# Performance work log

Measured on AMD Instinct MI355X. Metric: run time of the kernel, lower is better.

The kernel has to match this reference:

```python
import jax, jax.numpy as jnp
import numpy as np

DIM = 1024
HEADS = 16
DIM_HEAD = 64
INNER = HEADS * DIM_HEAD  # 1024
EPS = 1e-5


def setup_inputs() -> dict:
    key = jax.random.key(0)
    ks = jax.random.split(key, 8)
    B, N = 4, 2048
    s = 0.02
    return {
        "query": jax.random.normal(ks[0], (B, N, DIM), jnp.float32),
        "key_": jax.random.normal(ks[1], (B, N, DIM), jnp.float32),
        "value": jax.random.normal(ks[2], (B, N, DIM), jnp.float32),
        "Wq": jax.random.normal(ks[3], (DIM, INNER), jnp.float32) * s,
        "Wk": jax.random.normal(ks[4], (DIM, INNER), jnp.float32) * s,
        "Wv": jax.random.normal(ks[5], (DIM, INNER), jnp.float32) * s,
        "Wo": jax.random.normal(ks[6], (INNER, DIM), jnp.float32) * s,
        "bo": jnp.zeros((DIM,), jnp.float32),
        "gamma": jnp.ones((DIM,), jnp.float32),
        "beta": jnp.zeros((DIM,), jnp.float32),
    }


def reference(query, key_, value, Wq, Wk, Wv, Wo, bo, gamma, beta):
    B, N, _ = query.shape
    scale = DIM_HEAD ** (-0.5)
    # project and split heads: [B, H, N, Dh]
    q = (query @ Wq).reshape(B, N, HEADS, DIM_HEAD).transpose(0, 2, 1, 3)
    k = (key_ @ Wk).reshape(B, N, HEADS, DIM_HEAD).transpose(0, 2, 1, 3)
    v = (value @ Wv).reshape(B, N, HEADS, DIM_HEAD).transpose(0, 2, 1, 3)
    dots = jnp.einsum("bhnd,bhmd->bhnm", q, k) * scale  # [B,H,N,N]
    attn = jax.nn.softmax(dots, axis=-1)
    out = jnp.einsum("bhnm,bhmd->bhnd", attn, v)
    out = out.transpose(0, 2, 1, 3).reshape(B, N, INNER)
    out = out @ Wo + bo  # dropout p=0.0 is identity
    # LayerNorm over last dim
    mu = out.mean(-1, keepdims=True)
    var = ((out - mu) ** 2).mean(-1, keepdims=True)
    normed = (out - mu) * jax.lax.rsqrt(var + EPS) * gamma + beta
    return normed + query
```

## Files before the change

### kernel.cpp

```cpp
#include <hip/hip_runtime.h>
#include <stdint.h>

#define K_DIM 1024
#define B_SZ 4
#define N_SEQ 2048
#define HEADS 16
#define DH 64
#define M_TOT (B_SZ * N_SEQ)

typedef __bf16 bf16x8 __attribute__((ext_vector_type(8)));
typedef __bf16 bf16x4 __attribute__((ext_vector_type(4)));
typedef float f32x4 __attribute__((ext_vector_type(4)));

typedef const uint32_t __attribute__((address_space(1))) gas_u32;
typedef uint32_t __attribute__((address_space(3))) las_u32;

#define CE_SCALE 0.1803368801f

__device__ __forceinline__ uint16_t f2bf(float f) {
  uint32_t u = __float_as_uint(f);
  u += 0x7FFFu + ((u >> 16) & 1u);
  return (uint16_t)(u >> 16);
}

__device__ __forceinline__ void gld_lds16(const uint16_t* g, uint16_t* lds) {
  __builtin_amdgcn_global_load_lds((gas_u32*)g, (las_u32*)lds, 16, 0, 0);
}

__global__ __launch_bounds__(256) void conv_bf16_k(const float* __restrict__ s0,
                                                   const float* __restrict__ s1,
                                                   const float* __restrict__ s2,
                                                   uint16_t* __restrict__ dstbase, int n4) {
  const int z = blockIdx.y;
  const float* src = (z == 0) ? s0 : (z == 1) ? s1 : s2;
  uint16_t* dst = dstbase + (size_t)z * M_TOT * K_DIM;
  int i = blockIdx.x * blockDim.x + threadIdx.x;
  if (i < n4) {
    float4 v = ((const float4*)src)[i];
    ushort4 o;
    o.x = f2bf(v.x); o.y = f2bf(v.y); o.z = f2bf(v.z); o.w = f2bf(v.w);
    ((ushort4*)dst)[i] = o;
  }
}

__global__ __launch_bounds__(256) void transpose_conv(const float* __restrict__ s0,
                                                      const float* __restrict__ s1,
                                                      const float* __restrict__ s2,
                                                      const float* __restrict__ s3,
                                                      uint16_t* __restrict__ dstbase) {
  __shared__ float tile[32][33];
  const int z = blockIdx.z;
  const float* src = (z == 0) ? s0 : (z == 1) ? s1 : (z == 2) ? s2 : s3;
  uint16_t* dst = dstbase + (size_t)z * 1024 * 1024;
  const int tx = threadIdx.x, ty = threadIdx.y;
  const int bx = blockIdx.x * 32, by = blockIdx.y * 32;
#pragma unroll
  for (int i = 0; i < 32; i += 8)
    tile[ty + i][tx] = src[(size_t)(by + ty + i) * 1024 + bx + tx];
  __syncthreads();
#pragma unroll
  for (int i = 0; i < 32; i += 8)
    dst[(size_t)(bx + ty + i) * 1024 + by + tx] = f2bf(tile[tx][ty + i]);
}

template <int MODE>
__global__ __launch_bounds__(256, 2) void gemm_bf16(const uint16_t* __restrict__ A,
                                                    const uint16_t* __restrict__ BT,
                                                    void* __restrict__ Cout,
                                                    const float* __restrict__ bias) {
  __shared__ __align__(16) uint16_t As[128 * 32];
  __shared__ __align__(16) uint16_t Bs[128 * 32];
  const int tid = threadIdx.x;
  const int wave = tid >> 6, lane = tid & 63;
  const int g = lane >> 4, c16 = lane & 15;
  const int m0 = blockIdx.y * 128, n0 = blockIdx.x * 128;
  const int wr = wave >> 1, wc = wave & 1;
  float scale = 1.f;
  if (MODE == 0) {
    const int z = blockIdx.z;
    A += (size_t)z * M_TOT * K_DIM;
    BT += (size_t)z * 1024 * 1024;
    Cout = (void*)((uint16_t*)Cout + (size_t)z * M_TOT * K_DIM);
    scale = (z == 0) ? CE_SCALE : 1.f;
  }

  const f32x4 fzero = {0.f, 0.f, 0.f, 0.f};
  f32x4 acc[4][4];
#pragma unroll
  for (int i = 0; i < 4; ++i)
#pragma unroll
    for (int j = 0; j < 4; ++j) acc[i][j] = fzero;

  const int srow = wave * 32 + (lane >> 2);
  const int scol = (lane & 3) * 8;
  const uint16_t* ag0 = A + (size_t)(m0 + srow) * K_DIM + scol;
  const uint16_t* ag1 = A + (size_t)(m0 + srow + 16) * K_DIM + scol;
  const uint16_t* bg0 = BT + (size_t)(n0 + srow) * K_DIM + scol;
  const uint16_t* bg1 = BT + (size_t)(n0 + srow + 16) * K_DIM + scol;
  uint16_t* la0 = &As[(wave * 32) * 32];
  uint16_t* la1 = &As[(wave * 32 + 16) * 32];
  uint16_t* lb0 = &Bs[(wave * 32) * 32];
  uint16_t* lb1 = &Bs[(wave * 32 + 16) * 32];

  for (int kt = 0; kt < K_DIM / 32; ++kt) {
    __syncthreads();
    gld_lds16(ag0 + kt * 32, la0);
    gld_lds16(ag1 + kt * 32, la1);
    gld_lds16(bg0 + kt * 32, lb0);
    gld_lds16(bg1 + kt * 32, lb1);
    __syncthreads();
    bf16x8 avec[4], bvec[4];
#pragma unroll
    for (int i = 0; i < 4; ++i)
      avec[i] = *(const bf16x8*)&As[(wr * 64 + i * 16 + c16) * 32 + g * 8];
#pragma unroll
    for (int j = 0; j < 4; ++j)
      bvec[j] = *(const bf16x8*)&Bs[(wc * 64 + j * 16 + c16) * 32 + g * 8];
#pragma unroll
    for (int i = 0; i < 4; ++i)
#pragma unroll
      for (int j = 0; j < 4; ++j)
        acc[i][j] = __builtin_amdgcn_mfma_f32_16x16x32_bf16(avec[i], bvec[j], acc[i][j], 0, 0, 0);
  }

#pragma unroll
  for (int i = 0; i < 4; ++i) {
#pragma unroll
    for (int j = 0; j < 4; ++j) {
      const int col = n0 + wc * 64 + j * 16 + c16;
      if (MODE == 2) {
        const int h = col >> 6, d = col & 63;
        const int row0 = m0 + wr * 64 + i * 16 + g * 4;
        const int b = row0 >> 11, n = row0 & 2047;
        ushort4 o;
        o.x = f2bf(acc[i][j][0]); o.y = f2bf(acc[i][j][1]);
        o.z = f2bf(acc[i][j][2]); o.w = f2bf(acc[i][j][3]);
        *(ushort4*)&((uint16_t*)Cout)[(((size_t)(b * HEADS + h)) * DH + d) * N_SEQ + n] = o;
      } else {
#pragma unroll
        for (int r = 0; r < 4; ++r) {
          const int row = m0 + wr * 64 + i * 16 + g * 4 + r;
          if (MODE == 0) {
            const int b = row >> 11, n = row & 2047;
            const int h = col >> 6, d = col & 63;
            ((uint16_t*)Cout)[(((size_t)(b * HEADS + h)) * N_SEQ + n) * DH + d] =
                f2bf(acc[i][j][r] * scale);
          } else {
            ((float*)Cout)[(size_t)row * 1024 + col] = acc[i][j][r] + bias[col];
          }
        }
      }
    }
  }
}

__global__ __launch_bounds__(256, 4) void attention_k(const uint16_t* __restrict__ qm,
                                                      const uint16_t* __restrict__ km,
                                                      const uint16_t* __restrict__ vtm,
                                                      uint16_t* __restrict__ om) {
  __shared__ __align__(16) uint16_t Ks[64 * 64];
  __shared__ __align__(16) uint16_t Vs[64 * 64];
  __shared__ __align__(16) uint16_t Pt[4][32 * 64];
  const int tid = threadIdx.x;
  const int wave = tid >> 6, lane = tid & 63;
  const int g = lane >> 4, c16 = lane & 15;
  const int bh = blockIdx.y, b = bh >> 4, h = bh & 15;
  const int q0 = blockIdx.x * 128 + wave * 32;

  const uint16_t* qbase = qm + (size_t)bh * N_SEQ * DH;
  const uint16_t* kbase = km + (size_t)bh * N_SEQ * DH;
  const uint16_t* vbase = vtm + (size_t)bh * DH * N_SEQ;

  bf16x8 qf[2][2];
#pragma unroll
  for (int qc = 0; qc < 2; ++qc) {
    const uint16_t* qp = qbase + (size_t)(q0 + qc * 16 + c16) * DH + g * 8;
    qf[qc][0] = *(const bf16x8*)qp;
    qf[qc][1] = *(const bf16x8*)(qp + 32);
  }

  const f32x4 fz = {0.f, 0.f, 0.f, 0.f};
  f32x4 oacc[2][4];
#pragma unroll
  for (int qc = 0; qc < 2; ++qc)
#pragma unroll
    for (int jt = 0; jt < 4; ++jt) oacc[qc][jt] = fz;
  float l[2] = {0.f, 0.f};

  uint16_t* ptw = Pt[wave];
  const int sw = c16 & 7;

  for (int t = 0; t < N_SEQ / 64; ++t) {
    __syncthreads();
#pragma unroll
    for (int p = 0; p < 2; ++p) {
      const int idx = p * 256 + tid;
      {
        const int e = idx * 8, row = e >> 6, ch = idx & 7;
        *(uint4*)&Ks[row * 64 + ((ch ^ (row & 7)) << 3)] =
            *(const uint4*)&kbase[(size_t)t * 4096 + e];
      }
      {
        const int vr = idx >> 3, ch = idx & 7;
        *(uint4*)&Vs[vr * 64 + ((ch ^ (vr & 7)) << 3)] =
            *(const uint4*)&vbase[(size_t)vr * N_SEQ + t * 64 + ch * 8];
      }
    }
    __syncthreads();

#pragma unroll
    for (int kt = 0; kt < 4; ++kt) {
      const int krow = kt * 16 + c16;
      bf16x8 kf0 = *(const bf16x8*)&Ks[krow * 64 + ((g ^ sw) << 3)];
      bf16x8 kf1 = *(const bf16x8*)&Ks[krow * 64 + (((4 + g) ^ sw) << 3)];
#pragma unroll
      for (int qc = 0; qc < 2; ++qc) {
        f32x4 z = fz;
        z = __builtin_amdgcn_mfma_f32_16x16x32_bf16(kf0, qf[qc][0], z, 0, 0, 0);
        z = __builtin_amdgcn_mfma_f32_16x16x32_bf16(kf1, qf[qc][1], z, 0, 0, 0);
        const float p0 = __builtin_amdgcn_exp2f(z[0]);
        const float p1 = __builtin_amdgcn_exp2f(z[1]);
        const float p2 = __builtin_amdgcn_exp2f(z[2]);
        const float p3 = __builtin_amdgcn_exp2f(z[3]);
        l[qc] += (p0 + p1) + (p2 + p3);
        bf16x4 pk;
        pk[0] = (__bf16)p0; pk[1] = (__bf16)p1; pk[2] = (__bf16)p2; pk[3] = (__bf16)p3;
        *(bf16x4*)&ptw[(qc * 16 + c16) * 64 + (((kt * 2 + (g >> 1)) ^ sw) << 3) + (g & 1) * 4] = pk;
      }
    }

#pragma unroll
    for (int kc = 0; kc < 2; ++kc) {
      bf16x8 pa[2];
#pragma unroll
      for (int qc = 0; qc < 2; ++qc)
        pa[qc] = *(const bf16x8*)&ptw[(qc * 16 + c16) * 64 + (((kc * 4 + g) ^ sw) << 3)];
#pragma unroll
      for (int jt = 0; jt < 4; ++jt) {
        const int vrow = jt * 16 + c16;
        bf16x8 vb = *(const bf16x8*)&Vs[vrow * 64 + (((kc * 4 + g) ^ sw) << 3)];
#pragma unroll
        for (int qc = 0; qc < 2; ++qc)
          oacc[qc][jt] = __builtin_amdgcn_mfma_f32_16x16x32_bf16(pa[qc], vb, oacc[qc][jt], 0, 0, 0);
      }
    }
  }

#pragma unroll
  for (int qc = 0; qc < 2; ++qc) {
    l[qc] += __shfl_xor(l[qc], 16);
    l[qc] += __shfl_xor(l[qc], 32);
  }

#pragma unroll
  for (int qc = 0; qc < 2; ++qc) {
#pragma unroll
    for (int r = 0; r < 4; ++r) {
      const float lr = __shfl(l[qc], g * 4 + r, 16);
      const float inv = 1.f / lr;
      const int row = q0 + qc * 16 + g * 4 + r;
      const size_t base = ((size_t)b * N_SEQ + row) * 1024 + h * 64;
#pragma unroll
      for (int jt = 0; jt < 4; ++jt)
        om[base + jt * 16 + c16] = f2bf(oacc[qc][jt][r] * inv);
    }
  }
}

__global__ __launch_bounds__(256) void ln_res_k(const float* __restrict__ proj,
                                                const float* __restrict__ query,
                                                const float* __restrict__ gamma,
                                                const float* __restrict__ beta,
                                                float* __restrict__ out) {
  const int row = blockIdx.x;
  const int tid = threadIdx.x;
  const size_t base = (size_t)row * 1024 + tid * 4;
  float4 v = *(const float4*)(proj + base);
  float s = v.x + v.y + v.z + v.w;
  float s2 = v.x * v.x + v.y * v.y + v.z * v.z + v.w * v.w;
#pragma unroll
  for (int off = 1; off < 64; off <<= 1) {
    s += __shfl_xor(s, off);
    s2 += __shfl_xor(s2, off);
  }
  __shared__ float red[8];
  const int wave = tid >> 6, lane = tid & 63;
  if (lane == 0) { red[wave] = s; red[4 + wave] = s2; }
  __syncthreads();
  s = red[0] + red[1] + red[2] + red[3];
  s2 = red[4] + red[5] + red[6] + red[7];
  const float mu = s * (1.f / 1024.f);
  const float var = fmaxf(s2 * (1.f / 1024.f) - mu * mu, 0.f);
  const float rstd = rsqrtf(var + 1e-5f);
  float4 gq = *(const float4*)(gamma + tid * 4);
  float4 bq = *(const float4*)(beta + tid * 4);
  float4 qq = *(const float4*)(query + base);
  float4 o;
  o.x = (v.x - mu) * rstd * gq.x + bq.x + qq.x;
  o.y = (v.y - mu) * rstd * gq.y + bq.y + qq.y;
  o.z = (v.z - mu) * rstd * gq.z + bq.z + qq.z;
  o.w = (v.w - mu) * rstd * gq.w + bq.w + qq.w;
  *(float4*)(out + base) = o;
}

extern "C" void kernel_launch(void* const* d_in, const int* in_sizes, int n_in,
                              void* d_out, int out_size, void* d_ws, size_t ws_size,
                              hipStream_t stream) {
  (void)in_sizes; (void)n_in; (void)out_size; (void)ws_size;
  const float* query = (const float*)d_in[0];
  const float* key_ = (const float*)d_in[1];
  const float* value = (const float*)d_in[2];
  const float* Wq = (const float*)d_in[3];
  const float* Wk = (const float*)d_in[4];
  const float* Wv = (const float*)d_in[5];
  const float* Wo = (const float*)d_in[6];
  const float* bo = (const float*)d_in[7];
  const float* gamma = (const float*)d_in[8];
  const float* beta = (const float*)d_in[9];
  float* out = (float*)d_out;

  const size_t NELEM = (size_t)M_TOT * 1024;
  uint16_t* wsp = (uint16_t*)d_ws;
  uint16_t* WqT = wsp;
  uint16_t* WvT = WqT + 2 * 1024 * 1024;
  uint16_t* WoT = WqT + 3 * 1024 * 1024;
  uint16_t* xq = WqT + 4 * 1024 * 1024;
  uint16_t* xv = xq + 2 * NELEM;
  uint16_t* qb = xq + 3 * NELEM;
  uint16_t* vt = qb + 2 * NELEM;
  uint16_t* attnO = xq;
  float* proj = (float*)(xq + NELEM);

  const int n4 = (int)(NELEM / 4);
  conv_bf16_k<<<dim3(8192, 3), 256, 0, stream>>>(query, key_, value, xq, n4);

  transpose_conv<<<dim3(32, 32, 4), dim3(32, 8), 0, stream>>>(Wq, Wk, Wv, Wo, WqT);

  gemm_bf16<0><<<dim3(8, 64, 2), 256, 0, stream>>>(xq, WqT, qb, nullptr);
  gemm_bf16<2><<<dim3(8, 64), 256, 0, stream>>>(xv, WvT, vt, nullptr);

  attention_k<<<dim3(N_SEQ / 128, 64), 256, 0, stream>>>(qb, qb + NELEM, vt, attnO);

  gemm_bf16<1><<<dim3(8, 64), 256, 0, stream>>>(attnO, WoT, proj, bo);

  ln_res_k<<<8192, 256, 0, stream>>>(proj, query, gamma, beta, out);
}
```

Before: 374.2 us.

## Merge QKV projections into one launch and prefetch K/V tiles in attention

The Q, K and V projection GEMMs now run as a single launch with three z-slices, and V is written transposed from the third slice. This removes one kernel launch and its tail. The attention kernel now handles 64 query rows per wave (256 per block), so each K/V tile loaded into shared memory is reused across twice as many queries. It also prefetches the next K/V tile into registers during compute, which overlaps global loads with MFMA work. In exchange it uses more registers and shared memory, lowers launch bounds to 2 blocks per CU, and launches half as many attention blocks.

```diff
diff --git a/kernel.cpp b/kernel.cpp
--- a/kernel.cpp
+++ b/kernel.cpp
@@ -75,12 +75,12 @@
   const int g = lane >> 4, c16 = lane & 15;
   const int m0 = blockIdx.y * 128, n0 = blockIdx.x * 128;
   const int wr = wave >> 1, wc = wave & 1;
+  int z = 0;
   float scale = 1.f;
-  if (MODE == 0) {
-    const int z = blockIdx.z;
+  if (MODE == 3) {
+    z = blockIdx.z;
     A += (size_t)z * M_TOT * K_DIM;
     BT += (size_t)z * 1024 * 1024;
-    Cout = (void*)((uint16_t*)Cout + (size_t)z * M_TOT * K_DIM);
     scale = (z == 0) ? CE_SCALE : 1.f;
   }
 
@@ -128,22 +128,24 @@
 #pragma unroll
     for (int j = 0; j < 4; ++j) {
       const int col = n0 + wc * 64 + j * 16 + c16;
-      if (MODE == 2) {
+      if (MODE == 3 && z == 2) {
         const int h = col >> 6, d = col & 63;
         const int row0 = m0 + wr * 64 + i * 16 + g * 4;
         const int b = row0 >> 11, n = row0 & 2047;
         ushort4 o;
         o.x = f2bf(acc[i][j][0]); o.y = f2bf(acc[i][j][1]);
         o.z = f2bf(acc[i][j][2]); o.w = f2bf(acc[i][j][3]);
-        *(ushort4*)&((uint16_t*)Cout)[(((size_t)(b * HEADS + h)) * DH + d) * N_SEQ + n] = o;
+        *(ushort4*)&((uint16_t*)Cout)[(size_t)2 * M_TOT * 1024 +
+                                      (((size_t)(b * HEADS + h)) * DH + d) * N_SEQ + n] = o;
       } else {
 #pragma unroll
         for (int r = 0; r < 4; ++r) {
           const int row = m0 + wr * 64 + i * 16 + g * 4 + r;
-          if (MODE == 0) {
+          if (MODE == 3) {
             const int b = row >> 11, n = row & 2047;
             const int h = col >> 6, d = col & 63;
-            ((uint16_t*)Cout)[(((size_t)(b * HEADS + h)) * N_SEQ + n) * DH + d] =
+            ((uint16_t*)Cout)[(size_t)z * M_TOT * 1024 +
+                              (((size_t)(b * HEADS + h)) * N_SEQ + n) * DH + d] =
                 f2bf(acc[i][j][r] * scale);
           } else {
             ((float*)Cout)[(size_t)row * 1024 + col] = acc[i][j][r] + bias[col];
@@ -154,67 +156,76 @@
   }
 }
 
-__global__ __launch_bounds__(256, 4) void attention_k(const uint16_t* __restrict__ qm,
+__global__ __launch_bounds__(256, 2) void attention_k(const uint16_t* __restrict__ qm,
                                                       const uint16_t* __restrict__ km,
                                                       const uint16_t* __restrict__ vtm,
                                                       uint16_t* __restrict__ om) {
   __shared__ __align__(16) uint16_t Ks[64 * 64];
   __shared__ __align__(16) uint16_t Vs[64 * 64];
-  __shared__ __align__(16) uint16_t Pt[4][32 * 64];
+  __shared__ __align__(16) uint16_t Pt[4][64 * 64];
   const int tid = threadIdx.x;
   const int wave = tid >> 6, lane = tid & 63;
   const int g = lane >> 4, c16 = lane & 15;
   const int bh = blockIdx.y, b = bh >> 4, h = bh & 15;
-  const int q0 = blockIdx.x * 128 + wave * 32;
+  const int q0 = blockIdx.x * 256 + wave * 64;
 
   const uint16_t* qbase = qm + (size_t)bh * N_SEQ * DH;
   const uint16_t* kbase = km + (size_t)bh * N_SEQ * DH;
   const uint16_t* vbase = vtm + (size_t)bh * DH * N_SEQ;
 
-  bf16x8 qf[2][2];
-#pragma unroll
-  for (int qc = 0; qc < 2; ++qc) {
+  bf16x8 qf[4][2];
+#pragma unroll
+  for (int qc = 0; qc < 4; ++qc) {
     const uint16_t* qp = qbase + (size_t)(q0 + qc * 16 + c16) * DH + g * 8;
     qf[qc][0] = *(const bf16x8*)qp;
     qf[qc][1] = *(const bf16x8*)(qp + 32);
   }
 
   const f32x4 fz = {0.f, 0.f, 0.f, 0.f};
-  f32x4 oacc[2][4];
-#pragma unroll
-  for (int qc = 0; qc < 2; ++qc)
+  f32x4 oacc[4][4];
+#pragma unroll
+  for (int qc = 0; qc < 4; ++qc)
 #pragma unroll
     for (int jt = 0; jt < 4; ++jt) oacc[qc][jt] = fz;
-  float l[2] = {0.f, 0.f};
+  float l[4] = {0.f, 0.f, 0.f, 0.f};
 
   uint16_t* ptw = Pt[wave];
   const int sw = c16 & 7;
 
+  const int ch = tid & 7;
+  const int krow0 = tid >> 3, krow1 = (256 + tid) >> 3;
+  const int kdst0 = krow0 * 64 + ((ch ^ (krow0 & 7)) << 3);
+  const int kdst1 = krow1 * 64 + ((ch ^ (krow1 & 7)) << 3);
+
+  uint4 kp0, kp1, vp0, vp1;
+  kp0 = *(const uint4*)&kbase[(size_t)tid * 8];
+  kp1 = *(const uint4*)&kbase[(size_t)(256 + tid) * 8];
+  vp0 = *(const uint4*)&vbase[(size_t)krow0 * N_SEQ + ch * 8];
+  vp1 = *(const uint4*)&vbase[(size_t)krow1 * N_SEQ + ch * 8];
+  *(uint4*)&Ks[kdst0] = kp0;
+  *(uint4*)&Ks[kdst1] = kp1;
+  *(uint4*)&Vs[kdst0] = vp0;
+  *(uint4*)&Vs[kdst1] = vp1;
+  __syncthreads();
+
   for (int t = 0; t < N_SEQ / 64; ++t) {
-    __syncthreads();
-#pragma unroll
-    for (int p = 0; p < 2; ++p) {
-      const int idx = p * 256 + tid;
-      {
-        const int e = idx * 8, row = e >> 6, ch = idx & 7;
-        *(uint4*)&Ks[row * 64 + ((ch ^ (row & 7)) << 3)] =
-            *(const uint4*)&kbase[(size_t)t * 4096 + e];
-      }
-      {
-        const int vr = idx >> 3, ch = idx & 7;
-        *(uint4*)&Vs[vr * 64 + ((ch ^ (vr & 7)) << 3)] =
-            *(const uint4*)&vbase[(size_t)vr * N_SEQ + t * 64 + ch * 8];
-      }
-    }
-    __syncthreads();
+    if (t < N_SEQ / 64 - 1) {
+      const size_t ko = (size_t)(t + 1) * 4096;
+      const int vc = (t + 1) * 64;
+      kp0 = *(const uint4*)&kbase[ko + (size_t)tid * 8];
+      kp1 = *(const uint4*)&kbase[ko + (size_t)(256 + tid) * 8];
+      vp0 = *(const uint4*)&vbase[(size_t)krow0 * N_SEQ + vc + ch * 8];
+      vp1 = *(const uint4*)&vbase[(size_t)krow1 * N_SEQ + vc + ch * 8];
+    }
 
 #pragma unroll
     for (int kt = 0; kt < 4; ++kt) {
       const int krow = kt * 16 + c16;
       bf16x8 kf0 = *(const bf16x8*)&Ks[krow * 64 + ((g ^ sw) << 3)];
       bf16x8 kf1 = *(const bf16x8*)&Ks[krow * 64 + (((4 + g) ^ sw) << 3)];
-#pragma unroll
-      for (int qc = 0; qc < 2; ++qc) {
+      const int pcol = (((kt * 2 + (g >> 1)) ^ sw) << 3) + (g & 1) * 4;
+#pragma unroll
+      for (int qc = 0; qc < 4; ++qc) {
         f32x4 z = fz;
         z = __builtin_amdgcn_mfma_f32_16x16x32_bf16(kf0, qf[qc][0], z, 0, 0, 0);
         z = __builtin_amdgcn_mfma_f32_16x16x32_bf16(kf1, qf[qc][1], z, 0, 0, 0);
@@ -225,35 +236,44 @@
         l[qc] += (p0 + p1) + (p2 + p3);
         bf16x4 pk;
         pk[0] = (__bf16)p0; pk[1] = (__bf16)p1; pk[2] = (__bf16)p2; pk[3] = (__bf16)p3;
-        *(bf16x4*)&ptw[(qc * 16 + c16) * 64 + (((kt * 2 + (g >> 1)) ^ sw) << 3) + (g & 1) * 4] = pk;
+        *(bf16x4*)&ptw[(qc * 16 + c16) * 64 + pcol] = pk;
       }
     }
 
 #pragma unroll
     for (int kc = 0; kc < 2; ++kc) {
-      bf16x8 pa[2];
-#pragma unroll
-      for (int qc = 0; qc < 2; ++qc)
-        pa[qc] = *(const bf16x8*)&ptw[(qc * 16 + c16) * 64 + (((kc * 4 + g) ^ sw) << 3)];
+      const int fcol = ((kc * 4 + g) ^ sw) << 3;
+      bf16x8 pa[4];
+#pragma unroll
+      for (int qc = 0; qc < 4; ++qc)
+        pa[qc] = *(const bf16x8*)&ptw[(qc * 16 + c16) * 64 + fcol];
 #pragma unroll
       for (int jt = 0; jt < 4; ++jt) {
-        const int vrow = jt * 16 + c16;
-        bf16x8 vb = *(const bf16x8*)&Vs[vrow * 64 + (((kc * 4 + g) ^ sw) << 3)];
-#pragma unroll
-        for (int qc = 0; qc < 2; ++qc)
+        bf16x8 vb = *(const bf16x8*)&Vs[(jt * 16 + c16) * 64 + fcol];
+#pragma unroll
+        for (int qc = 0; qc < 4; ++qc)
           oacc[qc][jt] = __builtin_amdgcn_mfma_f32_16x16x32_bf16(pa[qc], vb, oacc[qc][jt], 0, 0, 0);
       }
     }
-  }
-
-#pragma unroll
-  for (int qc = 0; qc < 2; ++qc) {
+
+    if (t < N_SEQ / 64 - 1) {
+      __syncthreads();
+      *(uint4*)&Ks[kdst0] = kp0;
+      *(uint4*)&Ks[kdst1] = kp1;
+      *(uint4*)&Vs[kdst0] = vp0;
+      *(uint4*)&Vs[kdst1] = vp1;
+      __syncthreads();
+    }
+  }
+
+#pragma unroll
+  for (int qc = 0; qc < 4; ++qc) {
     l[qc] += __shfl_xor(l[qc], 16);
     l[qc] += __shfl_xor(l[qc], 32);
   }
 
 #pragma unroll
-  for (int qc = 0; qc < 2; ++qc) {
+  for (int qc = 0; qc < 4; ++qc) {
 #pragma unroll
     for (int r = 0; r < 4; ++r) {
       const float lr = __shfl(l[qc], g * 4 + r, 16);
@@ -322,12 +342,9 @@
   const size_t NELEM = (size_t)M_TOT * 1024;
   uint16_t* wsp = (uint16_t*)d_ws;
   uint16_t* WqT = wsp;
-  uint16_t* WvT = WqT + 2 * 1024 * 1024;
   uint16_t* WoT = WqT + 3 * 1024 * 1024;
   uint16_t* xq = WqT + 4 * 1024 * 1024;
-  uint16_t* xv = xq + 2 * NELEM;
   uint16_t* qb = xq + 3 * NELEM;
-  uint16_t* vt = qb + 2 * NELEM;
   uint16_t* attnO = xq;
   float* proj = (float*)(xq + NELEM);
 
@@ -336,10 +353,9 @@
 
   transpose_conv<<<dim3(32, 32, 4), dim3(32, 8), 0, stream>>>(Wq, Wk, Wv, Wo, WqT);
 
-  gemm_bf16<0><<<dim3(8, 64, 2), 256, 0, stream>>>(xq, WqT, qb, nullptr);
-  gemm_bf16<2><<<dim3(8, 64), 256, 0, stream>>>(xv, WvT, vt, nullptr);
-
-  attention_k<<<dim3(N_SEQ / 128, 64), 256, 0, stream>>>(qb, qb + NELEM, vt, attnO);
+  gemm_bf16<3><<<dim3(8, 64, 3), 256, 0, stream>>>(xq, WqT, qb, nullptr);
+
+  attention_k<<<dim3(N_SEQ / 256, 64), 256, 0, stream>>>(qb, qb + NELEM, qb + 2 * NELEM, attnO);
 
   gemm_bf16<1><<<dim3(8, 64), 256, 0, stream>>>(attnO, WoT, proj, bo);
 
```

Result: faster. 365.0 us (-2.4%).
